# Kernel tuning notes

Measured on AMD Instinct MI355X. Metric: run time of the kernel, lower is better.

## Reference

```python
import jax, jax.numpy as jnp
import numpy as np

B, S, HID, NH, AH, F = 1024, 100, 128, 2, 64, 2
DH = HID // NH          # item/pos head size = 64
DA = AH // NH           # attribute head size = 32
EPS = 1e-12


def setup_inputs() -> dict:
    key = jax.random.key(0)
    ks = iter(jax.random.split(key, 32))
    n = lambda shape, s=0.02: jax.random.normal(next(ks), shape, dtype=jnp.float32) * s
    inp = {
        "input_tensor": jax.random.normal(next(ks), (B, S, HID), dtype=jnp.float32),
        "attribute_table": jax.random.normal(next(ks), (F, B, S, AH), dtype=jnp.float32),
        "position_embedding": jax.random.normal(next(ks), (B, S, HID), dtype=jnp.float32),
        "attention_mask": jnp.zeros((B, 1, S, S), dtype=jnp.float32),
        # item / positional projections (stored [in, out])
        "Wq": n((HID, HID)), "bq": jnp.zeros((HID,), jnp.float32),
        "Wk": n((HID, HID)), "bk": jnp.zeros((HID,), jnp.float32),
        "Wv": n((HID, HID)), "bv": jnp.zeros((HID,), jnp.float32),
        "Wqp": n((HID, HID)), "bqp": jnp.zeros((HID,), jnp.float32),
        "Wkp": n((HID, HID)), "bkp": jnp.zeros((HID,), jnp.float32),
        # per-attribute projections, stacked over feat axis
        "Wq_attr": n((F, AH, AH)), "bq_attr": jnp.zeros((F, AH), jnp.float32),
        "Wk_attr": n((F, AH, AH)), "bk_attr": jnp.zeros((F, AH), jnp.float32),
        # gate fusion (VanillaAttentionX): Linear(S,S) -> ReLU -> Linear(S,1)
        "fuse_W1": n((S, S)), "fuse_b1": jnp.zeros((S,), jnp.float32),
        "fuse_W2": n((S, 1)), "fuse_b2": jnp.zeros((1,), jnp.float32),
        # output dense + LayerNorm
        "Wd": n((HID, HID)), "bd": jnp.zeros((HID,), jnp.float32),
        "ln_g": jnp.ones((HID,), jnp.float32), "ln_b": jnp.zeros((HID,), jnp.float32),
    }
    return inp


def _split_heads(x, nh):  # [B,S,nh*d] -> [B,nh,S,d]
    b, s, hd = x.shape
    return x.reshape(b, s, nh, hd // nh).transpose(0, 2, 1, 3)


def reference(input_tensor, attribute_table, position_embedding, attention_mask,
              Wq, bq, Wk, bk, Wv, bv, Wqp, bqp, Wkp, bkp,
              Wq_attr, bq_attr, Wk_attr, bk_attr,
              fuse_W1, fuse_b1, fuse_W2, fuse_b2,
              Wd, bd, ln_g, ln_b):
    b, s, hid = input_tensor.shape
    # item / positional QKV
    q = _split_heads(input_tensor @ Wq + bq, NH)
    k = _split_heads(input_tensor @ Wk + bk, NH)
    v = _split_heads(input_tensor @ Wv + bv, NH)
    qp = _split_heads(position_embedding @ Wqp + bqp, NH)
    kp = _split_heads(position_embedding @ Wkp + bkp, NH)
    item_scores = jnp.einsum('bhqd,bhkd->bhqk', q, k)
    pos_scores = jnp.einsum('bhqd,bhkd->bhqk', qp, kp)
    # attribute score streams: [F,B,S,AH] -> [F,B,NH,S,DA]
    aq = jnp.einsum('fbsa,fao->fbso', attribute_table, Wq_attr) + bq_attr[:, None, None, :]
    ak = jnp.einsum('fbsa,fao->fbso', attribute_table, Wk_attr) + bk_attr[:, None, None, :]
    aq = aq.reshape(F, b, s, NH, DA).transpose(0, 1, 3, 2, 4)
    ak = ak.reshape(F, b, s, NH, DA).transpose(0, 1, 3, 2, 4)
    attr_scores = jnp.einsum('fbhqd,fbhkd->fbhqk', aq, ak)  # [F,B,NH,S,S]
    # gate fusion: stack streams on axis -2 -> [B,NH,S,F+2,S]
    stacked = jnp.concatenate([
        jnp.moveaxis(attr_scores, 0, 3),
        item_scores[:, :, :, None, :],
        pos_scores[:, :, :, None, :],
    ], axis=-2)
    energy = jax.nn.relu(stacked @ fuse_W1 + fuse_b1) @ fuse_W2 + fuse_b2  # [B,NH,S,F+2,1]
    gate_w = jax.nn.softmax(energy[..., 0], axis=-1)                       # [B,NH,S,F+2]
    fused = jnp.einsum('bhsfk,bhsf->bhsk', stacked, gate_w)                # [B,NH,S,S]
    scores = fused / jnp.sqrt(jnp.asarray(DH, fused.dtype)) + attention_mask
    probs = jax.nn.softmax(scores, axis=-1)
    ctx = jnp.einsum('bhqk,bhkd->bhqd', probs, v)
    ctx = ctx.transpose(0, 2, 1, 3).reshape(b, s, hid)
    h = ctx @ Wd + bd + input_tensor
    mu = jnp.mean(h, axis=-1, keepdims=True)
    var = jnp.mean((h - mu) ** 2, axis=-1, keepdims=True)
    return (h - mu) / jnp.sqrt(var + EPS) * ln_g + ln_b
```

## Files before the change

### kernel.cpp

```cpp
#include <hip/hip_runtime.h>
#include <hip/hip_bf16.h>

using bf16 = __hip_bfloat16;
using u16 = unsigned short;
typedef __attribute__((ext_vector_type(8))) short bf16x8;
typedef __attribute__((ext_vector_type(16))) float f32x16;

namespace {

constexpr int B_  = 1024;
constexpr int Sd  = 100;
constexpr int BS_ = B_ * Sd;

constexpr int NTHR = 1024;
constexpr int NW   = 16;

constexpr int STP = 420;
constexpr int STS = 104;
constexpr int QKP = 196;
constexpr int AP  = 132;
constexpr int ATP = 68;
constexpr int W1P = 116;
constexpr int VTP = 116;

constexpr int O_ST = 0;
constexpr int O_Q  = 84000;
constexpr int O_K  = 123200;
constexpr int E2S  = 32000;
constexpr int LBYTES = 162400;

__device__ __forceinline__ float bfr(u16 u) {
  unsigned int x = ((unsigned int)u) << 16;
  float f; __builtin_memcpy(&f, &x, 4); return f;
}
__device__ __forceinline__ u16 f2bu(float x) {
  bf16 h = __float2bfloat16(x);
  u16 u; __builtin_memcpy(&u, &h, 2); return u;
}
__device__ __forceinline__ float4 ld4(const float* p) {
  return *reinterpret_cast<const float4*>(p);
}
__device__ __forceinline__ float wsum(float v) {
#pragma unroll
  for (int m = 32; m > 0; m >>= 1) v += __shfl_xor(v, m);
  return v;
}
__device__ __forceinline__ float wmax(float v) {
#pragma unroll
  for (int m = 32; m > 0; m >>= 1) v = fmaxf(v, __shfl_xor(v, m));
  return v;
}

__device__ __forceinline__ f32x16 zf16() {
  f32x16 z;
#pragma unroll
  for (int i = 0; i < 16; ++i) z[i] = 0.f;
  return z;
}
__device__ __forceinline__ f32x16 MFMA32(bf16x8 a, bf16x8 b, f32x16 c) {
  return __builtin_amdgcn_mfma_f32_32x32x16_bf16(a, b, c, 0, 0, 0);
}

__device__ __forceinline__ bf16x8 ld8(const u16* p) {
  const ushort4 a = *reinterpret_cast<const ushort4*>(p);
  const ushort4 b = *reinterpret_cast<const ushort4*>(p + 4);
  bf16x8 f;
  f[0] = (short)a.x; f[1] = (short)a.y; f[2] = (short)a.z; f[3] = (short)a.w;
  f[4] = (short)b.x; f[5] = (short)b.y; f[6] = (short)b.z; f[7] = (short)b.w;
  return f;
}

template <int L4>
__device__ __forceinline__ void stage_rows4(const float* __restrict__ src, u16* dst,
                                            int nrow, int pitch, int tid, int nthr) {
  for (int i = tid; i < (nrow << L4); i += nthr) {
    const int rr = i >> L4, cc = (i & ((1 << L4) - 1)) << 2;
    const float4 v = *reinterpret_cast<const float4*>(src + ((size_t)rr << (L4 + 2)) + cc);
    ushort4 o;
    o.x = f2bu(v.x); o.y = f2bu(v.y); o.z = f2bu(v.z); o.w = f2bu(v.w);
    *reinterpret_cast<ushort4*>(dst + rr * pitch + cc) = o;
  }
}
template <int LC>
__device__ __forceinline__ void stage_wt(const float* __restrict__ W, int ldw, int coff,
                                         u16* dst, int kd, int pitch, int tid, int nthr) {
  constexpr int NC = 1 << LC;
  for (int idx = tid; idx < NC * kd; idx += nthr) {
    const int k = idx >> LC, c = idx & (NC - 1);
    dst[c * pitch + k] = f2bu(W[k * ldw + coff + c]);
  }
}

template <int KD, bool TR>
__device__ __forceinline__ void tile32(const u16* A, int apitch, const u16* Wt, int wpitch,
                                       const float* __restrict__ bias, u16* dst, int dpitch,
                                       int dbase, int m0, int n0, int l) {
  const int cr = l & 31, g = l >> 5;
  int ar = m0 + cr; if (ar >= Sd) ar = Sd - 1;
  const u16* ap = A + ar * apitch + g * 8;
  const u16* bp = Wt + (n0 + cr) * wpitch + g * 8;
  f32x16 acc = zf16();
#pragma unroll
  for (int k0 = 0; k0 < KD; k0 += 16)
    acc = MFMA32(ld8(ap + k0), ld8(bp + k0), acc);
  const float bvv = bias[n0 + cr];
#pragma unroll
  for (int i = 0; i < 16; ++i) {
    const int row = m0 + (i & 3) + 8 * (i >> 2) + 4 * g;
    if (row < Sd) {
      if (TR) dst[(n0 + cr) * dpitch + dbase + row] = f2bu(acc[i] + bvv);
      else    dst[row * dpitch + dbase + n0 + cr]   = f2bu(acc[i] + bvv);
    }
  }
}

__global__ __launch_bounds__(NTHR) void attn_mega(
    const float* __restrict__ input, const float* __restrict__ attrT,
    const float* __restrict__ posE, const float* __restrict__ mask,
    const float* __restrict__ Wq, const float* __restrict__ bq,
    const float* __restrict__ Wk, const float* __restrict__ bk,
    const float* __restrict__ Wv, const float* __restrict__ bv,
    const float* __restrict__ Wqp, const float* __restrict__ bqp,
    const float* __restrict__ Wkp, const float* __restrict__ bkp,
    const float* __restrict__ Wqa, const float* __restrict__ bqa,
    const float* __restrict__ Wka, const float* __restrict__ bka,
    const float* __restrict__ W1, const float* __restrict__ b1,
    const float* __restrict__ W2, float* __restrict__ ctx) {
  __shared__ __align__(16) char L[LBYTES];
  u16* const ST = (u16*)(L + O_ST);
  u16* const QC = (u16*)(L + O_Q);
  u16* const KC = (u16*)(L + O_K);
  u16* const SA  = (u16*)(L + O_ST);
  u16* const SW1 = (u16*)(L + O_ST + 26400);
  u16* const SW2 = (u16*)(L + O_ST + 43296);
  u16* const AT0  = (u16*)(L + O_ST);
  u16* const AT1  = (u16*)(L + O_ST + 13600);
  u16* const WA0Q = (u16*)(L + O_ST + 27200);
  u16* const WA0K = (u16*)(L + O_ST + 31552);
  u16* const WA1Q = (u16*)(L + O_ST + 35904);
  u16* const WA1K = (u16*)(L + O_ST + 40256);
  u16* const W1T = (u16*)(L + O_K);
  float* const e2s = (float*)(L + O_K + E2S);
  u16* const VA  = (u16*)(L + O_Q);
  u16* const WVT = (u16*)(L + O_K);
  u16* const VT  = (u16*)(L + O_K + 16896);

  const int tid = threadIdx.x;
  const int bh = blockIdx.x;
  const int b = bh >> 1, h = bh & 1;
  const size_t row0 = (size_t)b * Sd;
  const int l = tid & 63, w = tid >> 6;
  const int cr = l & 31, g = l >> 5;

  stage_rows4<5>(input + row0 * 128, SA, 100, AP, tid, NTHR);
  stage_wt<6>(Wq, 128, h * 64, SW1, 128, AP, tid, NTHR);
  stage_wt<6>(Wk, 128, h * 64, SW2, 128, AP, tid, NTHR);
  float4 r2[8];
#pragma unroll
  for (int s = 0; s < 8; ++s) {
    const int fi = tid + s * NTHR;
    if (fi < 3200) {
      r2[s] = ld4(posE + row0 * 128 + fi * 4);
    } else if (fi < 5248) {
      const int f2 = fi - 3200, k = f2 >> 4, c0 = (f2 & 15) << 2;
      r2[s] = ld4(Wqp + k * 128 + h * 64 + c0);
    } else if (fi < 7296) {
      const int f2 = fi - 5248, k = f2 >> 4, c0 = (f2 & 15) << 2;
      r2[s] = ld4(Wkp + k * 128 + h * 64 + c0);
    }
  }
  __syncthreads();

  {
    const int pr = w >> 3, mt = (w >> 1) & 3, nt = w & 1;
    tile32<128, false>(SA, AP, pr ? SW2 : SW1, AP, (pr ? bk : bq) + h * 64,
                       pr ? KC : QC, QKP, 0, mt * 32, nt * 32, l);
  }
  __syncthreads();

#pragma unroll
  for (int s = 0; s < 8; ++s) {
    const int fi = tid + s * NTHR;
    if (fi < 3200) {
      ushort4 o;
      o.x = f2bu(r2[s].x); o.y = f2bu(r2[s].y); o.z = f2bu(r2[s].z); o.w = f2bu(r2[s].w);
      *reinterpret_cast<ushort4*>(SA + (fi >> 5) * AP + ((fi & 31) << 2)) = o;
    } else if (fi < 5248) {
      const int f2 = fi - 3200, k = f2 >> 4, c0 = (f2 & 15) << 2;
      SW1[c0 * AP + k] = f2bu(r2[s].x); SW1[(c0 + 1) * AP + k] = f2bu(r2[s].y);
      SW1[(c0 + 2) * AP + k] = f2bu(r2[s].z); SW1[(c0 + 3) * AP + k] = f2bu(r2[s].w);
    } else if (fi < 7296) {
      const int f2 = fi - 5248, k = f2 >> 4, c0 = (f2 & 15) << 2;
      SW2[c0 * AP + k] = f2bu(r2[s].x); SW2[(c0 + 1) * AP + k] = f2bu(r2[s].y);
      SW2[(c0 + 2) * AP + k] = f2bu(r2[s].z); SW2[(c0 + 3) * AP + k] = f2bu(r2[s].w);
    }
  }
  float4 r3[6];
#pragma unroll
  for (int s = 0; s < 6; ++s) {
    const int fi = tid + s * NTHR;
    if (fi < 1600) {
      r3[s] = ld4(attrT + (size_t)b * 6400 + fi * 4);
    } else if (fi < 3200) {
      r3[s] = ld4(attrT + (size_t)(B_ + b) * 6400 + (fi - 1600) * 4);
    } else if (fi < 5248) {
      const int f3 = fi - 3200, which = f3 >> 9, fj = f3 & 511;
      const int k = fj >> 3, c0 = (fj & 7) << 2;
      const float* src = (which == 0) ? Wqa : (which == 1) ? Wka
                       : (which == 2) ? (Wqa + 4096) : (Wka + 4096);
      r3[s] = ld4(src + k * 64 + h * 32 + c0);
    }
  }
  __syncthreads();

  {
    const int pr = w >> 3, mt = (w >> 1) & 3, nt = w & 1;
    tile32<128, false>(SA, AP, pr ? SW2 : SW1, AP, (pr ? bkp : bqp) + h * 64,
                       pr ? KC : QC, QKP, 64, mt * 32, nt * 32, l);
  }
  __syncthreads();

#pragma unroll
  for (int s = 0; s < 6; ++s) {
    const int fi = tid + s * NTHR;
    if (fi < 1600) {
      ushort4 o;
      o.x = f2bu(r3[s].x); o.y = f2bu(r3[s].y); o.z = f2bu(r3[s].z); o.w = f2bu(r3[s].w);
      *reinterpret_cast<ushort4*>(AT0 + (fi >> 4) * ATP + ((fi & 15) << 2)) = o;
    } else if (fi < 3200) {
      const int f3 = fi - 1600;
      ushort4 o;
      o.x = f2bu(r3[s].x); o.y = f2bu(r3[s].y); o.z = f2bu(r3[s].z); o.w = f2bu(r3[s].w);
      *reinterpret_cast<ushort4*>(AT1 + (f3 >> 4) * ATP + ((f3 & 15) << 2)) = o;
    } else if (fi < 5248) {
      const int f3 = fi - 3200, which = f3 >> 9, fj = f3 & 511;
      const int k = fj >> 3, c0 = (fj & 7) << 2;
      u16* dst = (which == 0) ? WA0Q : (which == 1) ? WA0K
               : (which == 2) ? WA1Q : WA1K;
      dst[c0 * ATP + k] = f2bu(r3[s].x); dst[(c0 + 1) * ATP + k] = f2bu(r3[s].y);
      dst[(c0 + 2) * ATP + k] = f2bu(r3[s].z); dst[(c0 + 3) * ATP + k] = f2bu(r3[s].w);
    }
  }
  float4 r5[3];
#pragma unroll
  for (int s = 0; s < 3; ++s) {
    const int fi = tid + s * NTHR;
    if (fi < 2500) r5[s] = ld4(W1 + fi * 4);
  }
  __syncthreads();

  {
    const int pr = w >> 2, mt = w & 3;
    const u16* Asrc = (pr < 2) ? AT0 : AT1;
    const u16* Wt = (pr == 0) ? WA0Q : (pr == 1) ? WA0K : (pr == 2) ? WA1Q : WA1K;
    const float* bs = (pr == 0) ? bqa + h * 32 : (pr == 1) ? bka + h * 32
                     : (pr == 2) ? bqa + 64 + h * 32 : bka + 64 + h * 32;
    tile32<64, false>(Asrc, ATP, Wt, ATP, bs, (pr & 1) ? KC : QC, QKP,
                      128 + (pr >> 1) * 32, mt * 32, 0, l);
  }
  __syncthreads();

  {
    ushort4 z; z.x = z.y = z.z = z.w = 0;
    for (int q = tid; q < Sd; q += NTHR)
      *reinterpret_cast<ushort4*>(ST + q * STP + 416) = z;
  }
  {
    const int mt = w >> 2, nt = w & 3;
    const int m0 = mt * 32, n0 = nt * 32;
    int ar = m0 + cr; if (ar >= Sd) ar = Sd - 1;
    int br = n0 + cr; if (br >= Sd) br = Sd - 1;
    const u16* ap = QC + ar * QKP + g * 8;
    const u16* bp = KC + br * QKP + g * 8;
    f32x16 ai = zf16(), po = zf16(), a0 = zf16(), a1 = zf16();
    ai = MFMA32(ld8(ap + 0),   ld8(bp + 0),   ai);
    ai = MFMA32(ld8(ap + 16),  ld8(bp + 16),  ai);
    ai = MFMA32(ld8(ap + 32),  ld8(bp + 32),  ai);
    ai = MFMA32(ld8(ap + 48),  ld8(bp + 48),  ai);
    po = MFMA32(ld8(ap + 64),  ld8(bp + 64),  po);
    po = MFMA32(ld8(ap + 80),  ld8(bp + 80),  po);
    po = MFMA32(ld8(ap + 96),  ld8(bp + 96),  po);
    po = MFMA32(ld8(ap + 112), ld8(bp + 112), po);
    a0 = MFMA32(ld8(ap + 128), ld8(bp + 128), a0);
    a0 = MFMA32(ld8(ap + 144), ld8(bp + 144), a0);
    a1 = MFMA32(ld8(ap + 160), ld8(bp + 160), a1);
    a1 = MFMA32(ld8(ap + 176), ld8(bp + 176), a1);
    const int col = n0 + cr;
    if (col < STS) {
#pragma unroll
      for (int i = 0; i < 16; ++i) {
        const int row = m0 + (i & 3) + 8 * (i >> 2) + 4 * g;
        if (row < Sd) {
          u16* sp = ST + row * STP + col;
          sp[0]       = f2bu(a0[i]);
          sp[STS]     = f2bu(a1[i]);
          sp[2 * STS] = f2bu(ai[i]);
          sp[3 * STS] = f2bu(po[i]);
        }
      }
    }
  }
  __syncthreads();

  {
    ushort4 z; z.x = z.y = z.z = z.w = 0;
    if (tid < 812)
      *reinterpret_cast<ushort4*>(W1T + 11600 + tid * 4) = z;
    if (tid < 400) {
      const int c = tid >> 2, kq = 100 + ((tid & 3) << 2);
      *reinterpret_cast<ushort4*>(W1T + c * W1P + kq) = z;
    }
  }
#pragma unroll
  for (int s = 0; s < 3; ++s) {
    const int fi = tid + s * NTHR;
    if (fi < 2500) {
#pragma unroll
      for (int j = 0; j < 4; ++j) {
        const int o = fi * 4 + j;
        const int k = o / 100, c = o - k * 100;
        W1T[c * W1P + k] = f2bu((j == 0) ? r5[s].x : (j == 1) ? r5[s].y
                                : (j == 2) ? r5[s].z : r5[s].w);
      }
    }
  }
  __syncthreads();

  {
    float b1v[4], w2v[4];
#pragma unroll
    for (int nt = 0; nt < 4; ++nt) {
      const int c = nt * 32 + cr;
      b1v[nt] = (c < Sd) ? b1[c] : 0.f;
      w2v[nt] = (c < Sd) ? W2[c] : 0.f;
    }
    for (int mt = w; mt < 13; mt += NW) {
      const int m0 = mt * 32;
      int gr = m0 + cr; if (gr > 399) gr = 399;
      const u16* ap = ST + (gr >> 2) * STP + (gr & 3) * STS + g * 8;
      f32x16 c0 = zf16(), c1 = zf16(), c2 = zf16(), c3 = zf16();
#pragma unroll
      for (int k0 = 0; k0 < 112; k0 += 16) {
        const bf16x8 af = ld8(ap + k0);
        c0 = MFMA32(af, ld8(W1T + (cr)      * W1P + g * 8 + k0), c0);
        c1 = MFMA32(af, ld8(W1T + (32 + cr) * W1P + g * 8 + k0), c1);
        c2 = MFMA32(af, ld8(W1T + (64 + cr) * W1P + g * 8 + k0), c2);
        c3 = MFMA32(af, ld8(W1T + (96 + cr) * W1P + g * 8 + k0), c3);
      }
#pragma unroll
      for (int i = 0; i < 16; ++i) {
        float v = fmaxf(c0[i] + b1v[0], 0.f) * w2v[0]
                + fmaxf(c1[i] + b1v[1], 0.f) * w2v[1]
                + fmaxf(c2[i] + b1v[2], 0.f) * w2v[2]
                + fmaxf(c3[i] + b1v[3], 0.f) * w2v[3];
#pragma unroll
        for (int mm = 1; mm < 32; mm <<= 1) v += __shfl_xor(v, mm);
        if (cr == 0) {
          const int go = m0 + (i & 3) + 8 * (i >> 2) + 4 * g;
          if (go < 400) e2s[go] = v;
        }
      }
    }
  }
  __syncthreads();

  stage_rows4<5>(input + row0 * 128, VA, 100, AP, tid, NTHR);
  stage_wt<6>(Wv, 128, h * 64, WVT, 128, AP, tid, NTHR);
  {
    ushort4 z; z.x = z.y = z.z = z.w = 0;
    for (int i2 = tid; i2 < 64 * VTP / 4; i2 += NTHR)
      *reinterpret_cast<ushort4*>(VT + i2 * 4) = z;
  }
  for (int q = w; q < Sd; q += NW) {
    const float* ez = e2s + q * 4;
    float e0 = ez[0], e1 = ez[1], e2v = ez[2], e3 = ez[3];
    const float mg = fmaxf(fmaxf(e0, e1), fmaxf(e2v, e3));
    e0 = __expf(e0 - mg); e1 = __expf(e1 - mg);
    e2v = __expf(e2v - mg); e3 = __expf(e3 - mg);
    const float ginv = 1.0f / (e0 + e1 + e2v + e3);
    const float g0v = e0 * ginv, g1v = e1 * ginv, g2v = e2v * ginv, g3v = e3 * ginv;
    u16* const sp = ST + q * STP;
    const float* const mp = mask + (size_t)b * 10000 + q * 100;
    float x1 = g0v * bfr(sp[l]) + g1v * bfr(sp[STS + l]) +
               g2v * bfr(sp[2 * STS + l]) + g3v * bfr(sp[3 * STS + l]);
    x1 = x1 * 0.125f + mp[l];
    const bool v2 = (l < 36);
    float x2 = -3e38f;
    if (v2) {
      const int k2 = 64 + l;
      x2 = g0v * bfr(sp[k2]) + g1v * bfr(sp[STS + k2]) +
           g2v * bfr(sp[2 * STS + k2]) + g3v * bfr(sp[3 * STS + k2]);
      x2 = x2 * 0.125f + mp[k2];
    }
    const float M = wmax(fmaxf(x1, x2));
    const float ea = __expf(x1 - M);
    const float eb = v2 ? __expf(x2 - M) : 0.f;
    const float inv = 1.0f / wsum(ea + eb);
    sp[l] = f2bu(ea * inv);
    if (v2) sp[64 + l] = f2bu(eb * inv);
  }
  __syncthreads();

  if (w < 8) {
    const int mt = w >> 1, nt = w & 1;
    tile32<128, true>(VA, AP, WVT, AP, bv + h * 64, VT, VTP, 0, mt * 32, nt * 32, l);
  }
  __syncthreads();

  if (w < 8) {
    const int mt = w >> 1, nt = w & 1;
    const int m0 = mt * 32, n0 = nt * 32;
    int ar = m0 + cr; if (ar >= Sd) ar = Sd - 1;
    const u16* ap = ST + ar * STP + g * 8;
    const u16* bp = VT + (n0 + cr) * VTP + g * 8;
    f32x16 acc = zf16();
#pragma unroll
    for (int k0 = 0; k0 < 112; k0 += 16)
      acc = MFMA32(ld8(ap + k0), ld8(bp + k0), acc);
#pragma unroll
    for (int i = 0; i < 16; ++i) {
      const int row = m0 + (i & 3) + 8 * (i >> 2) + 4 * g;
      if (row < Sd)
        ctx[(row0 + row) * 128 + h * 64 + n0 + cr] = acc[i];
    }
  }
}

__global__ __launch_bounds__(512) void dense_ln(
    const float* __restrict__ ctxg, const float* __restrict__ Wd,
    const float* __restrict__ bd, const float* __restrict__ resid,
    const float* __restrict__ lng, const float* __restrict__ lnb,
    float* __restrict__ out) {
  __shared__ __align__(16) char L[101376];
  u16* const Ab  = (u16*)L;
  u16* const WdT = (u16*)(L + 33792);
  u16* const Hs  = (u16*)(L + 67584);
  const int tid = threadIdx.x;
  const size_t row0 = (size_t)blockIdx.x * 128;
  const int l = tid & 63, w = tid >> 6, cr = l & 31, g = l >> 5;

  stage_rows4<5>(ctxg + row0 * 128, Ab, 128, AP, tid, 512);
  stage_wt<7>(Wd, 128, 0, WdT, 128, AP, tid, 512);
  __syncthreads();

  for (int u = w; u < 16; u += 8) {
    const int m0 = (u >> 2) * 32, n0 = (u & 3) * 32;
    const u16* ap = Ab + (m0 + cr) * AP + g * 8;
    const u16* bp = WdT + (n0 + cr) * AP + g * 8;
    f32x16 acc = zf16();
#pragma unroll
    for (int k0 = 0; k0 < 128; k0 += 16)
      acc = MFMA32(ld8(ap + k0), ld8(bp + k0), acc);
#pragma unroll
    for (int i = 0; i < 16; ++i) {
      const int row = m0 + (i & 3) + 8 * (i >> 2) + 4 * g;
      Hs[row * AP + n0 + cr] = f2bu(acc[i]);
    }
  }
  __syncthreads();

  for (int rr = w; rr < 128; rr += 8) {
    const size_t grow = row0 + rr;
    const float h1 = bfr(Hs[rr * AP + l])      + bd[l]      + resid[grow * 128 + l];
    const float h2 = bfr(Hs[rr * AP + 64 + l]) + bd[64 + l] + resid[grow * 128 + 64 + l];
    const float mu = wsum(h1 + h2) * (1.0f / 128.0f);
    const float d1 = h1 - mu, d2 = h2 - mu;
    const float var = wsum(d1 * d1 + d2 * d2) * (1.0f / 128.0f);
    const float rs = rsqrtf(var + 1e-12f);
    out[grow * 128 + l]      = d1 * rs * lng[l]      + lnb[l];
    out[grow * 128 + 64 + l] = d2 * rs * lng[64 + l] + lnb[64 + l];
  }
}

}

extern "C" void kernel_launch(void* const* d_in, const int* in_sizes, int n_in,
                              void* d_out, int out_size, void* d_ws,
                              size_t ws_size, hipStream_t stream) {
  (void)in_sizes; (void)n_in; (void)out_size; (void)d_ws; (void)ws_size;

  const float* input = (const float*)d_in[0];
  const float* attrT = (const float*)d_in[1];
  const float* posE  = (const float*)d_in[2];
  const float* mask  = (const float*)d_in[3];
  const float* Wq  = (const float*)d_in[4];  const float* bq  = (const float*)d_in[5];
  const float* Wk  = (const float*)d_in[6];  const float* bk  = (const float*)d_in[7];
  const float* Wv  = (const float*)d_in[8];  const float* bv  = (const float*)d_in[9];
  const float* Wqp = (const float*)d_in[10]; const float* bqp = (const float*)d_in[11];
  const float* Wkp = (const float*)d_in[12]; const float* bkp = (const float*)d_in[13];
  const float* Wqa = (const float*)d_in[14]; const float* bqa = (const float*)d_in[15];
  const float* Wka = (const float*)d_in[16]; const float* bka = (const float*)d_in[17];
  const float* W1  = (const float*)d_in[18]; const float* b1  = (const float*)d_in[19];
  const float* W2  = (const float*)d_in[20];
  const float* Wd  = (const float*)d_in[22]; const float* bd  = (const float*)d_in[23];
  const float* lng = (const float*)d_in[24]; const float* lnb = (const float*)d_in[25];

  float* ctx = (float*)d_out;

  attn_mega<<<dim3(B_ * 2), dim3(NTHR), 0, stream>>>(
      input, attrT, posE, mask, Wq, bq, Wk, bk, Wv, bv, Wqp, bqp, Wkp, bkp,
      Wqa, bqa, Wka, bka, W1, b1, W2, ctx);
  dense_ln<<<dim3(BS_ / 128), dim3(512), 0, stream>>>(
      ctx, Wd, bd, input, lng, lnb, ctx);
}
```

Measured before the change: 325.2 us.

## Pre-convert and pre-transpose weights to bf16 once in a workspace prep kernel

Adds a small prep kernel that converts all projection, attribute, gate and dense weights to bf16 in the transposed layout the main kernels want, and stores them in the workspace. The attention and dense kernels then fill shared memory with vectorized ushort4 copies instead of strided fp32 loads, per-element conversion and scattered transposed LDS writes in every block. This cuts redundant per-block global traffic and conversion work. The cost is one extra launch and a dependence on the workspace being large enough, with a fallback to the old path otherwise.

```diff
diff --git a/kernel.cpp b/kernel.cpp
--- a/kernel.cpp
+++ b/kernel.cpp
@@ -28,6 +28,16 @@
 constexpr int O_K  = 123200;
 constexpr int E2S  = 32000;
 constexpr int LBYTES = 162400;
+
+constexpr int WQT_E  = 0;
+constexpr int WKT_E  = 16384;
+constexpr int WQPT_E = 32768;
+constexpr int WKPT_E = 49152;
+constexpr int WVT_E  = 65536;
+constexpr int WAT_E  = 81920;
+constexpr int W1T_E  = 98304;
+constexpr int WDT_E  = 113152;
+constexpr size_t WS_NEED = 129536ull * 2;
 
 __device__ __forceinline__ float bfr(u16 u) {
   unsigned int x = ((unsigned int)u) << 16;
@@ -90,6 +100,14 @@
     dst[c * pitch + k] = f2bu(W[k * ldw + coff + c]);
   }
 }
+__device__ __forceinline__ void copy_w64(const u16* __restrict__ src, u16* dst,
+                                         int tid, int nthr) {
+  for (int i = tid; i < 2048; i += nthr) {
+    const int r = i >> 5, c4 = (i & 31) << 2;
+    *reinterpret_cast<ushort4*>(dst + r * AP + c4) =
+        *reinterpret_cast<const ushort4*>(src + r * 128 + c4);
+  }
+}
 
 template <int KD, bool TR>
 __device__ __forceinline__ void tile32(const u16* A, int apitch, const u16* Wt, int wpitch,
@@ -114,6 +132,40 @@
   }
 }
 
+__global__ __launch_bounds__(256) void prep_weights(
+    const float* __restrict__ Wq, const float* __restrict__ Wk,
+    const float* __restrict__ Wqp, const float* __restrict__ Wkp,
+    const float* __restrict__ Wv, const float* __restrict__ Wqa,
+    const float* __restrict__ Wka, const float* __restrict__ W1,
+    const float* __restrict__ Wd, u16* __restrict__ ws) {
+  const int t = blockIdx.x * 256 + threadIdx.x;
+  const int NT = gridDim.x * 256;
+  const float* srcs[5] = {Wq, Wk, Wqp, Wkp, Wv};
+#pragma unroll
+  for (int wsel = 0; wsel < 5; ++wsel) {
+    u16* dst = ws + wsel * 16384;
+    const float* src = srcs[wsel];
+    for (int i = t; i < 16384; i += NT) {
+      const int h = i >> 13, c = (i >> 7) & 63, k = i & 127;
+      dst[i] = f2bu(src[k * 128 + h * 64 + c]);
+    }
+  }
+  for (int i = t; i < 16384; i += NT) {
+    const int pr = i >> 12, h = (i >> 11) & 1, c = (i >> 6) & 31, k = i & 63;
+    const float* src = (pr & 1) ? Wka : Wqa;
+    ws[WAT_E + i] = f2bu(src[(pr >> 1) * 4096 + k * 64 + h * 32 + c]);
+  }
+  for (int i = t; i < 14848; i += NT) {
+    const int c = i / W1P, k = i - c * W1P;
+    ws[W1T_E + i] = (c < Sd && k < Sd) ? f2bu(W1[k * Sd + c]) : (u16)0;
+  }
+  for (int i = t; i < 16384; i += NT) {
+    const int c = i >> 7, k = i & 127;
+    ws[WDT_E + i] = f2bu(Wd[k * 128 + c]);
+  }
+}
+
+template <bool PREP>
 __global__ __launch_bounds__(NTHR) void attn_mega(
     const float* __restrict__ input, const float* __restrict__ attrT,
     const float* __restrict__ posE, const float* __restrict__ mask,
@@ -125,7 +177,8 @@
     const float* __restrict__ Wqa, const float* __restrict__ bqa,
     const float* __restrict__ Wka, const float* __restrict__ bka,
     const float* __restrict__ W1, const float* __restrict__ b1,
-    const float* __restrict__ W2, float* __restrict__ ctx) {
+    const float* __restrict__ W2, const u16* __restrict__ wsw,
+    float* __restrict__ ctx) {
   __shared__ __align__(16) char L[LBYTES];
   u16* const ST = (u16*)(L + O_ST);
   u16* const QC = (u16*)(L + O_Q);
@@ -153,18 +206,24 @@
   const int cr = l & 31, g = l >> 5;
 
   stage_rows4<5>(input + row0 * 128, SA, 100, AP, tid, NTHR);
-  stage_wt<6>(Wq, 128, h * 64, SW1, 128, AP, tid, NTHR);
-  stage_wt<6>(Wk, 128, h * 64, SW2, 128, AP, tid, NTHR);
+  if constexpr (PREP) {
+    copy_w64(wsw + WQT_E + h * 8192, SW1, tid, NTHR);
+    copy_w64(wsw + WKT_E + h * 8192, SW2, tid, NTHR);
+  } else {
+    stage_wt<6>(Wq, 128, h * 64, SW1, 128, AP, tid, NTHR);
+    stage_wt<6>(Wk, 128, h * 64, SW2, 128, AP, tid, NTHR);
+  }
   float4 r2[8];
 #pragma unroll
   for (int s = 0; s < 8; ++s) {
+    if (PREP && s >= 4) break;
     const int fi = tid + s * NTHR;
     if (fi < 3200) {
       r2[s] = ld4(posE + row0 * 128 + fi * 4);
-    } else if (fi < 5248) {
+    } else if (!PREP && fi < 5248) {
       const int f2 = fi - 3200, k = f2 >> 4, c0 = (f2 & 15) << 2;
       r2[s] = ld4(Wqp + k * 128 + h * 64 + c0);
-    } else if (fi < 7296) {
+    } else if (!PREP && fi < 7296) {
       const int f2 = fi - 5248, k = f2 >> 4, c0 = (f2 & 15) << 2;
       r2[s] = ld4(Wkp + k * 128 + h * 64 + c0);
     }
@@ -180,30 +239,36 @@
 
 #pragma unroll
   for (int s = 0; s < 8; ++s) {
+    if (PREP && s >= 4) break;
     const int fi = tid + s * NTHR;
     if (fi < 3200) {
       ushort4 o;
       o.x = f2bu(r2[s].x); o.y = f2bu(r2[s].y); o.z = f2bu(r2[s].z); o.w = f2bu(r2[s].w);
       *reinterpret_cast<ushort4*>(SA + (fi >> 5) * AP + ((fi & 31) << 2)) = o;
-    } else if (fi < 5248) {
+    } else if (!PREP && fi < 5248) {
       const int f2 = fi - 3200, k = f2 >> 4, c0 = (f2 & 15) << 2;
       SW1[c0 * AP + k] = f2bu(r2[s].x); SW1[(c0 + 1) * AP + k] = f2bu(r2[s].y);
       SW1[(c0 + 2) * AP + k] = f2bu(r2[s].z); SW1[(c0 + 3) * AP + k] = f2bu(r2[s].w);
-    } else if (fi < 7296) {
+    } else if (!PREP && fi < 7296) {
       const int f2 = fi - 5248, k = f2 >> 4, c0 = (f2 & 15) << 2;
       SW2[c0 * AP + k] = f2bu(r2[s].x); SW2[(c0 + 1) * AP + k] = f2bu(r2[s].y);
       SW2[(c0 + 2) * AP + k] = f2bu(r2[s].z); SW2[(c0 + 3) * AP + k] = f2bu(r2[s].w);
     }
   }
+  if constexpr (PREP) {
+    copy_w64(wsw + WQPT_E + h * 8192, SW1, tid, NTHR);
+    copy_w64(wsw + WKPT_E + h * 8192, SW2, tid, NTHR);
+  }
   float4 r3[6];
 #pragma unroll
   for (int s = 0; s < 6; ++s) {
+    if (PREP && s >= 4) break;
     const int fi = tid + s * NTHR;
     if (fi < 1600) {
       r3[s] = ld4(attrT + (size_t)b * 6400 + fi * 4);
     } else if (fi < 3200) {
       r3[s] = ld4(attrT + (size_t)(B_ + b) * 6400 + (fi - 1600) * 4);
-    } else if (fi < 5248) {
+    } else if (!PREP && fi < 5248) {
       const int f3 = fi - 3200, which = f3 >> 9, fj = f3 & 511;
       const int k = fj >> 3, c0 = (fj & 7) << 2;
       const float* src = (which == 0) ? Wqa : (which == 1) ? Wka
@@ -222,6 +287,7 @@
 
 #pragma unroll
   for (int s = 0; s < 6; ++s) {
+    if (PREP && s >= 4) break;
     const int fi = tid + s * NTHR;
     if (fi < 1600) {
       ushort4 o;
@@ -232,7 +298,7 @@
       ushort4 o;
       o.x = f2bu(r3[s].x); o.y = f2bu(r3[s].y); o.z = f2bu(r3[s].z); o.w = f2bu(r3[s].w);
       *reinterpret_cast<ushort4*>(AT1 + (f3 >> 4) * ATP + ((f3 & 15) << 2)) = o;
-    } else if (fi < 5248) {
+    } else if (!PREP && fi < 5248) {
       const int f3 = fi - 3200, which = f3 >> 9, fj = f3 & 511;
       const int k = fj >> 3, c0 = (fj & 7) << 2;
       u16* dst = (which == 0) ? WA0Q : (which == 1) ? WA0K
@@ -241,11 +307,28 @@
       dst[(c0 + 2) * ATP + k] = f2bu(r3[s].z); dst[(c0 + 3) * ATP + k] = f2bu(r3[s].w);
     }
   }
+  if constexpr (PREP) {
+    for (int i = tid; i < 2048; i += NTHR) {
+      const int pr = i >> 9, row = (i >> 4) & 31, c4 = (i & 15) << 2;
+      u16* dst = (pr == 0) ? WA0Q : (pr == 1) ? WA0K : (pr == 2) ? WA1Q : WA1K;
+      *reinterpret_cast<ushort4*>(dst + row * ATP + c4) =
+          *reinterpret_cast<const ushort4*>(wsw + WAT_E + pr * 4096 + h * 2048 + row * 64 + c4);
+    }
+  }
   float4 r5[3];
-#pragma unroll
-  for (int s = 0; s < 3; ++s) {
-    const int fi = tid + s * NTHR;
-    if (fi < 2500) r5[s] = ld4(W1 + fi * 4);
+  ushort4 rw1[4];
+  if constexpr (PREP) {
+#pragma unroll
+    for (int s = 0; s < 4; ++s) {
+      const int fi = tid + s * NTHR;
+      if (fi < 3712) rw1[s] = reinterpret_cast<const ushort4*>(wsw + W1T_E)[fi];
+    }
+  } else {
+#pragma unroll
+    for (int s = 0; s < 3; ++s) {
+      const int fi = tid + s * NTHR;
+      if (fi < 2500) r5[s] = ld4(W1 + fi * 4);
+    }
   }
   __syncthreads();
 
@@ -302,25 +385,33 @@
   }
   __syncthreads();
 
-  {
-    ushort4 z; z.x = z.y = z.z = z.w = 0;
-    if (tid < 812)
-      *reinterpret_cast<ushort4*>(W1T + 11600 + tid * 4) = z;
-    if (tid < 400) {
-      const int c = tid >> 2, kq = 100 + ((tid & 3) << 2);
-      *reinterpret_cast<ushort4*>(W1T + c * W1P + kq) = z;
-    }
-  }
-#pragma unroll
-  for (int s = 0; s < 3; ++s) {
-    const int fi = tid + s * NTHR;
-    if (fi < 2500) {
-#pragma unroll
-      for (int j = 0; j < 4; ++j) {
-        const int o = fi * 4 + j;
-        const int k = o / 100, c = o - k * 100;
-        W1T[c * W1P + k] = f2bu((j == 0) ? r5[s].x : (j == 1) ? r5[s].y
-                                : (j == 2) ? r5[s].z : r5[s].w);
+  if constexpr (PREP) {
+#pragma unroll
+    for (int s = 0; s < 4; ++s) {
+      const int fi = tid + s * NTHR;
+      if (fi < 3712) reinterpret_cast<ushort4*>(W1T)[fi] = rw1[s];
+    }
+  } else {
+    {
+      ushort4 z; z.x = z.y = z.z = z.w = 0;
+      if (tid < 812)
+        *reinterpret_cast<ushort4*>(W1T + 11600 + tid * 4) = z;
+      if (tid < 400) {
+        const int c = tid >> 2, kq = 100 + ((tid & 3) << 2);
+        *reinterpret_cast<ushort4*>(W1T + c * W1P + kq) = z;
+      }
+    }
+#pragma unroll
+    for (int s = 0; s < 3; ++s) {
+      const int fi = tid + s * NTHR;
+      if (fi < 2500) {
+#pragma unroll
+        for (int j = 0; j < 4; ++j) {
+          const int o = fi * 4 + j;
+          const int k = o / 100, c = o - k * 100;
+          W1T[c * W1P + k] = f2bu((j == 0) ? r5[s].x : (j == 1) ? r5[s].y
+                                  : (j == 2) ? r5[s].z : r5[s].w);
+        }
       }
     }
   }
@@ -365,7 +456,11 @@
   __syncthreads();
 
   stage_rows4<5>(input + row0 * 128, VA, 100, AP, tid, NTHR);
-  stage_wt<6>(Wv, 128, h * 64, WVT, 128, AP, tid, NTHR);
+  if constexpr (PREP) {
+    copy_w64(wsw + WVT_E + h * 8192, WVT, tid, NTHR);
+  } else {
+    stage_wt<6>(Wv, 128, h * 64, WVT, 128, AP, tid, NTHR);
+  }
   {
     ushort4 z; z.x = z.y = z.z = z.w = 0;
     for (int i2 = tid; i2 < 64 * VTP / 4; i2 += NTHR)
@@ -426,11 +521,12 @@
   }
 }
 
+template <bool PREP>
 __global__ __launch_bounds__(512) void dense_ln(
     const float* __restrict__ ctxg, const float* __restrict__ Wd,
     const float* __restrict__ bd, const float* __restrict__ resid,
     const float* __restrict__ lng, const float* __restrict__ lnb,
-    float* __restrict__ out) {
+    const u16* __restrict__ wsw, float* __restrict__ out) {
   __shared__ __align__(16) char L[101376];
   u16* const Ab  = (u16*)L;
   u16* const WdT = (u16*)(L + 33792);
@@ -440,7 +536,15 @@
   const int l = tid & 63, w = tid >> 6, cr = l & 31, g = l >> 5;
 
   stage_rows4<5>(ctxg + row0 * 128, Ab, 128, AP, tid, 512);
-  stage_wt<7>(Wd, 128, 0, WdT, 128, AP, tid, 512);
+  if constexpr (PREP) {
+    for (int i = tid; i < 4096; i += 512) {
+      const int r = i >> 5, c4 = (i & 31) << 2;
+      *reinterpret_cast<ushort4*>(WdT + r * AP + c4) =
+          *reinterpret_cast<const ushort4*>(wsw + WDT_E + r * 128 + c4);
+    }
+  } else {
+    stage_wt<7>(Wd, 128, 0, WdT, 128, AP, tid, 512);
+  }
   __syncthreads();
 
   for (int u = w; u < 16; u += 8) {
@@ -477,7 +581,7 @@
 extern "C" void kernel_launch(void* const* d_in, const int* in_sizes, int n_in,
                               void* d_out, int out_size, void* d_ws,
                               size_t ws_size, hipStream_t stream) {
-  (void)in_sizes; (void)n_in; (void)out_size; (void)d_ws; (void)ws_size;
+  (void)in_sizes; (void)n_in; (void)out_size;
 
   const float* input = (const float*)d_in[0];
   const float* attrT = (const float*)d_in[1];
@@ -497,9 +601,20 @@
 
   float* ctx = (float*)d_out;
 
-  attn_mega<<<dim3(B_ * 2), dim3(NTHR), 0, stream>>>(
-      input, attrT, posE, mask, Wq, bq, Wk, bk, Wv, bv, Wqp, bqp, Wkp, bkp,
-      Wqa, bqa, Wka, bka, W1, b1, W2, ctx);
-  dense_ln<<<dim3(BS_ / 128), dim3(512), 0, stream>>>(
-      ctx, Wd, bd, input, lng, lnb, ctx);
-}
+  if (ws_size >= WS_NEED) {
+    u16* wsw = (u16*)d_ws;
+    prep_weights<<<dim3(128), dim3(256), 0, stream>>>(
+        Wq, Wk, Wqp, Wkp, Wv, Wqa, Wka, W1, Wd, wsw);
+    attn_mega<true><<<dim3(B_ * 2), dim3(NTHR), 0, stream>>>(
+        input, attrT, posE, mask, Wq, bq, Wk, bk, Wv, bv, Wqp, bqp, Wkp, bkp,
+        Wqa, bqa, Wka, bka, W1, b1, W2, wsw, ctx);
+    dense_ln<true><<<dim3(BS_ / 128), dim3(512), 0, stream>>>(
+        ctx, Wd, bd, input, lng, lnb, wsw, ctx);
+  } else {
+    attn_mega<false><<<dim3(B_ * 2), dim3(NTHR), 0, stream>>>(
+        input, attrT, posE, mask, Wq, bq, Wk, bk, Wv, bv, Wqp, bqp, Wkp, bkp,
+        Wqa, bqa, Wka, bka, W1, b1, W2, nullptr, ctx);
+    dense_ln<false><<<dim3(BS_ / 128), dim3(512), 0, stream>>>(
+        ctx, Wd, bd, input, lng, lnb, nullptr, ctx);
+  }
+}
```

Measured after the change: 326.6 us. Within noise of the previous version (+0.4%).
